# Performance work log

Measured on AMD Instinct MI355X. Metric: run time of the kernel, lower is better.

## Reference

```python
import jax, jax.numpy as jnp
import numpy as np

DIM = 1024
HEADS = 16
DH = DIM // HEADS          # 64
ROT_DIM = 2 * DH           # 128, rotary applied over concatenated x/a head dim
B, N = 2, 2048


def l2norm(t, eps=1e-12):
    # F.normalize(p=2, dim=-1)
    n = jnp.sqrt(jnp.sum(t * t, axis=-1, keepdims=True))
    return t / jnp.maximum(n, eps)


def rotate_half(t):
    t1, t2 = jnp.split(t, 2, axis=-1)
    return jnp.concatenate([-t2, t1], axis=-1)


def apply_rotary(q, k):
    # q: [b,h,n,ROT_DIM], k: [b,1,n,ROT_DIM]
    n = q.shape[-2]
    inv_freq = 1.0 / (10000.0 ** (jnp.arange(0, ROT_DIM, 2, dtype=jnp.float32) / ROT_DIM))
    freqs = jnp.outer(jnp.arange(n, dtype=jnp.float32), inv_freq)  # [n, ROT_DIM/2]
    emb = jnp.concatenate([freqs, freqs], axis=-1)                 # [n, ROT_DIM]
    cos, sin = jnp.cos(emb), jnp.sin(emb)
    q = q * cos + rotate_half(q) * sin
    k = k * cos + rotate_half(k) * sin
    return q, k


def setup_inputs() -> dict:
    key = jax.random.key(0)
    ks = jax.random.split(key, 6)
    s = 0.02
    return {
        "x": jax.random.normal(ks[0], (B, N, DIM), jnp.float32),
        "a": jax.random.normal(ks[1], (B, N, DIM), jnp.float32),
        "Wq_x": jax.random.normal(ks[2], (DIM, DIM), jnp.float32) * s,
        "Wkv_x": jax.random.normal(ks[3], (2 * DH, DIM), jnp.float32) * s,
        "Wq_a": jax.random.normal(ks[4], (DIM, DIM), jnp.float32) * s,
        "Wkv_a": jax.random.normal(ks[5], (2 * DH, DIM), jnp.float32) * s,
        "qx_scale": jnp.ones((HEADS, 1, DH), jnp.float32),
        "qa_scale": jnp.ones((HEADS, 1, DH), jnp.float32),
        "kx_scale": jnp.ones((1, 1, DH), jnp.float32),
        "ka_scale": jnp.ones((1, 1, DH), jnp.float32),
    }


def reference(x, a, Wq_x, Wkv_x, Wq_a, Wkv_a, qx_scale, qa_scale, kx_scale, ka_scale):
    b, n, _ = x.shape
    # q projections: [b,n,dim] -> [b,h,n,dh]
    q_x = (x @ Wq_x.T).reshape(b, n, HEADS, DH).transpose(0, 2, 1, 3)
    q_a = (a @ Wq_a.T).reshape(b, n, HEADS, DH).transpose(0, 2, 1, 3)
    # shared single KV head: [b,n,2*dh] -> two [b,1,n,dh]
    kv_x = x @ Wkv_x.T
    k_x, v_x = jnp.split(kv_x[:, None], 2, axis=-1)
    kv_a = a @ Wkv_a.T
    k_a, v_a = jnp.split(kv_a[:, None], 2, axis=-1)
    # qk-norm with learned per-head (q) / shared (k) scales
    q_x = l2norm(q_x) * qx_scale
    q_a = l2norm(q_a) * qa_scale
    k_x = l2norm(k_x) * kx_scale
    k_a = l2norm(k_a) * ka_scale
    # concat modalities along feature dim -> head dim 2*dh
    q = jnp.concatenate([q_x, q_a], axis=-1)   # [b,h,n,2dh]
    k = jnp.concatenate([k_x, k_a], axis=-1)   # [b,1,n,2dh]
    v = jnp.concatenate([v_x, v_a], axis=-1)   # [b,1,n,2dh]
    q, k = apply_rotary(q, k)
    # SDPA with broadcasted single KV head
    scale = 1.0 / jnp.sqrt(jnp.float32(ROT_DIM))
    k2, v2 = k[:, 0], v[:, 0]                  # [b,n,2dh]
    scores = jnp.einsum("bhqd,bkd->bhqk", q * scale, k2)
    attn = jax.nn.softmax(scores, axis=-1)
    out = jnp.einsum("bhqk,bkd->bhqd", attn, v2)  # [b,h,n,2dh]
    return out.transpose(0, 2, 1, 3).reshape(b, n, HEADS * ROT_DIM)
```

## Files before the change

kernel.cpp:

```cpp
#include <hip/hip_runtime.h>
#include <math.h>

#define DIM   1024
#define HEADS 16
#define DH    64
#define ROT   128
#define BATCH 2
#define SEQ   2048
#define ROWS  (BATCH*SEQ)
#define PCOLS (DIM + 2*DH)
#define ASCALE (0.08838834764831845f * 1.4426950408889634f)

typedef short bf16x8 __attribute__((ext_vector_type(8)));
typedef float f32x16 __attribute__((ext_vector_type(16)));
typedef unsigned u32x2 __attribute__((ext_vector_type(2)));

static __device__ __forceinline__ unsigned short f2bf(float f) {
    union { float f; unsigned u; } v; v.f = f;
    unsigned r = v.u + 0x7fffu + ((v.u >> 16) & 1u);
    return (unsigned short)(r >> 16);
}
static __device__ __forceinline__ float bf2f(unsigned short u) {
    union { unsigned u; float f; } v; v.u = (unsigned)u << 16;
    return v.f;
}

#define GL2LDS(gp, lp) __builtin_amdgcn_global_load_lds(                    \
    (const __attribute__((address_space(1))) void*)(gp),                    \
    (__attribute__((address_space(3))) void*)(lp), 16, 0, 0)
#define CFENCE() asm volatile("" ::: "memory")
#define WAIT_VM8()  __builtin_amdgcn_s_waitcnt(0xF78)
#define WAIT_VM0()  __builtin_amdgcn_s_waitcnt(0xF70)

__global__ __launch_bounds__(256) void convert_kernel(
    const float* __restrict__ x, const float* __restrict__ a,
    const float* __restrict__ Wq_x, const float* __restrict__ Wkv_x,
    const float* __restrict__ Wq_a, const float* __restrict__ Wkv_a,
    unsigned short* __restrict__ xbf, unsigned short* __restrict__ wbf,
    float2* __restrict__ tbl)
{
    const int blk = blockIdx.x;
    const float LN1E4_64 = 0.14391156831213f;
    if (blk >= 2624) {
        int local = blk - 2624;
        int pos = local * 16 + (threadIdx.x >> 4);
        int i   = threadIdx.x & 15;
        #pragma unroll
        for (int j = 0; j < 4; j++) {
            int jd = i * 4 + j;
            float th = (float)pos * expf(-LN1E4_64 * (float)jd);
            float sn, cs; sincosf(th, &sn, &cs);
            tbl[pos * 64 + jd] = make_float2(cs, sn);
        }
        return;
    }
    const float* s; unsigned short* d; int seg0;
    if      (blk < 1024) { s = x;     d = xbf;           seg0 = 0;    }
    else if (blk < 2048) { s = a;     d = xbf + 4194304; seg0 = 1024; }
    else if (blk < 2304) { s = Wq_x;  d = wbf;           seg0 = 2048; }
    else if (blk < 2336) { s = Wkv_x; d = wbf + 1048576; seg0 = 2304; }
    else if (blk < 2592) { s = Wq_a;  d = wbf + 1179648; seg0 = 2336; }
    else                 { s = Wkv_a; d = wbf + 2228224; seg0 = 2592; }
    long lb = ((long)blk - seg0) * 1024;
    #pragma unroll
    for (int j = 0; j < 4; j++) {
        long idx = lb + j * 256 + threadIdx.x;
        float4 v = ((const float4*)s)[idx];
        ((ushort4*)d)[idx] = make_ushort4(f2bf(v.x), f2bf(v.y), f2bf(v.z), f2bf(v.w));
    }
}

__global__ __launch_bounds__(256) void mfma_gemm_kernel(
    const unsigned short* __restrict__ xbf, const unsigned short* __restrict__ wbf,
    unsigned short* __restrict__ Pbf)
{
    const int mt = blockIdx.x, jt = blockIdx.y, side = blockIdx.z;
    const unsigned short* Ag = xbf + ((size_t)side * ROWS  + mt * 128) * DIM;
    const unsigned short* Bg = wbf + ((size_t)side * PCOLS + jt * 128) * DIM;
    unsigned short* Pp = Pbf + (size_t)side * ROWS * PCOLS;

    __shared__ __align__(16) unsigned short As[128 * 32];
    __shared__ __align__(16) unsigned short Bs[128 * 32];

    const int tid  = threadIdx.x;
    const int wave = tid >> 6, lane = tid & 63;
    const int m = lane & 31, hl = lane >> 5;
    const int wr = wave >> 1, wc = wave & 1;

    f32x16 acc[2][2];
    #pragma unroll
    for (int i2 = 0; i2 < 2; i2++)
        #pragma unroll
        for (int j2 = 0; j2 < 2; j2++) acc[i2][j2] = 0.0f;

    int sr[2], sg[2]; unsigned ldsb[2];
    #pragma unroll
    for (int it = 0; it < 2; it++) {
        int s = it * 256 + tid;
        sr[it] = s >> 2;
        sg[it] = (s & 3) ^ ((sr[it] >> 1) & 3);
        ldsb[it] = (unsigned)(it * 256 + wave * 64) * 16;
    }

    for (int k0 = 0; k0 < DIM; k0 += 32) {
        __syncthreads();
        #pragma unroll
        for (int it = 0; it < 2; it++) {
            GL2LDS(Ag + (size_t)sr[it] * DIM + k0 + sg[it] * 8, (char*)As + ldsb[it]);
            GL2LDS(Bg + (size_t)sr[it] * DIM + k0 + sg[it] * 8, (char*)Bs + ldsb[it]);
        }
        __syncthreads();
        #pragma unroll
        for (int kp = 0; kp < 2; kp++) {
            bf16x8 af[2], bff[2];
            #pragma unroll
            for (int t2 = 0; t2 < 2; t2++) {
                int ra = wr * 64 + t2 * 32 + m;
                int ga = (kp * 2 + hl) ^ ((ra >> 1) & 3);
                af[t2] = *(const bf16x8*)&As[ra * 32 + ga * 8];
                int rb = wc * 64 + t2 * 32 + m;
                int gb = (kp * 2 + hl) ^ ((rb >> 1) & 3);
                bff[t2] = *(const bf16x8*)&Bs[rb * 32 + gb * 8];
            }
            #pragma unroll
            for (int i2 = 0; i2 < 2; i2++)
                #pragma unroll
                for (int j2 = 0; j2 < 2; j2++)
                    acc[i2][j2] = __builtin_amdgcn_mfma_f32_32x32x16_bf16(
                        af[i2], bff[j2], acc[i2][j2], 0, 0, 0);
        }
    }

    const int m0 = mt * 128 + wr * 64;
    const int n0 = jt * 128 + wc * 64;
    #pragma unroll
    for (int i2 = 0; i2 < 2; i2++)
        #pragma unroll
        for (int j2 = 0; j2 < 2; j2++)
            #pragma unroll
            for (int r = 0; r < 16; r++) {
                int row = m0 + i2 * 32 + (r & 3) + 8 * (r >> 2) + 4 * hl;
                int col = n0 + j2 * 32 + m;
                Pp[(size_t)row * PCOLS + col] = f2bf(acc[i2][j2][r]);
            }
}

__global__ __launch_bounds__(256) void fuse_kernel(
    const unsigned short* __restrict__ Pbf,
    const float* __restrict__ qx_scale, const float* __restrict__ qa_scale,
    const float* __restrict__ kx_scale, const float* __restrict__ ka_scale,
    const float2* __restrict__ tbl,
    unsigned short* __restrict__ qbuf, unsigned short* __restrict__ kbuf,
    unsigned short* __restrict__ vbufT)
{
    const int row = blockIdx.x;
    const int b = row >> 11, pos = row & 2047;
    const unsigned short* Px = Pbf + (size_t)row * PCOLS;
    const unsigned short* Pa = Pbf + (size_t)ROWS * PCOLS + (size_t)row * PCOLS;
    const int tid = threadIdx.x;
    const int h = tid >> 4, i = tid & 15;
    const float2* tb = tbl + pos * 64;

    ushort4 xu = *(const ushort4*)(Px + h * DH + i * 4);
    ushort4 au = *(const ushort4*)(Pa + h * DH + i * 4);
    float xr[4] = {bf2f(xu.x), bf2f(xu.y), bf2f(xu.z), bf2f(xu.w)};
    float ar[4] = {bf2f(au.x), bf2f(au.y), bf2f(au.z), bf2f(au.w)};
    float ssx = xr[0]*xr[0] + xr[1]*xr[1] + xr[2]*xr[2] + xr[3]*xr[3];
    float ssa = ar[0]*ar[0] + ar[1]*ar[1] + ar[2]*ar[2] + ar[3]*ar[3];
    #pragma unroll
    for (int off = 1; off < 16; off <<= 1) {
        ssx += __shfl_xor(ssx, off, 16);
        ssa += __shfl_xor(ssa, off, 16);
    }
    float inx = 1.0f / fmaxf(sqrtf(ssx), 1e-12f);
    float ina = 1.0f / fmaxf(sqrtf(ssa), 1e-12f);
    unsigned short qlo[4], qhi[4];
    #pragma unroll
    for (int j = 0; j < 4; j++) {
        int jd = i * 4 + j;
        float qx = xr[j] * inx * qx_scale[h * DH + jd];
        float qa = ar[j] * ina * qa_scale[h * DH + jd];
        float2 cssn = tb[jd];
        qlo[j] = f2bf((qx * cssn.x - qa * cssn.y) * ASCALE);
        qhi[j] = f2bf((qa * cssn.x + qx * cssn.y) * ASCALE);
    }
    unsigned short* qp = qbuf + (((size_t)(b * HEADS + h)) * SEQ + pos) * ROT;
    *(ushort4*)(qp + i * 4)      = make_ushort4(qlo[0], qlo[1], qlo[2], qlo[3]);
    *(ushort4*)(qp + DH + i * 4) = make_ushort4(qhi[0], qhi[1], qhi[2], qhi[3]);

    if (tid < 16) {
        ushort4 kxu = *(const ushort4*)(Px + DIM + tid * 4);
        ushort4 kau = *(const ushort4*)(Pa + DIM + tid * 4);
        float kxr[4] = {bf2f(kxu.x), bf2f(kxu.y), bf2f(kxu.z), bf2f(kxu.w)};
        float kar[4] = {bf2f(kau.x), bf2f(kau.y), bf2f(kau.z), bf2f(kau.w)};
        float sx = kxr[0]*kxr[0] + kxr[1]*kxr[1] + kxr[2]*kxr[2] + kxr[3]*kxr[3];
        float sa = kar[0]*kar[0] + kar[1]*kar[1] + kar[2]*kar[2] + kar[3]*kar[3];
        #pragma unroll
        for (int off = 1; off < 16; off <<= 1) {
            sx += __shfl_xor(sx, off, 16);
            sa += __shfl_xor(sa, off, 16);
        }
        float ikx = 1.0f / fmaxf(sqrtf(sx), 1e-12f);
        float ika = 1.0f / fmaxf(sqrtf(sa), 1e-12f);
        unsigned short klo[4], khi[4];
        #pragma unroll
        for (int j = 0; j < 4; j++) {
            int jd = tid * 4 + j;
            float kx = kxr[j] * ikx * kx_scale[jd];
            float ka = kar[j] * ika * ka_scale[jd];
            float2 cssn = tb[jd];
            klo[j] = f2bf(kx * cssn.x - ka * cssn.y);
            khi[j] = f2bf(ka * cssn.x + kx * cssn.y);
        }
        unsigned short* kp = kbuf + ((size_t)b * SEQ + pos) * ROT;
        *(ushort4*)(kp + tid * 4)      = make_ushort4(klo[0], klo[1], klo[2], klo[3]);
        *(ushort4*)(kp + DH + tid * 4) = make_ushort4(khi[0], khi[1], khi[2], khi[3]);
    }
    if (tid >= 64 && tid < 96) {
        int iv = tid - 64;
        unsigned short* vT = vbufT + (size_t)b * ROT * SEQ + pos;
        const unsigned short* src; int d;
        if (iv < 16) { src = Px + DIM + DH + iv * 4;        d = iv * 4;              }
        else         { src = Pa + DIM + DH + (iv - 16) * 4; d = DH + (iv - 16) * 4;  }
        ushort4 v4 = *(const ushort4*)src;
        vT[(size_t)(d + 0) * SEQ] = v4.x;
        vT[(size_t)(d + 1) * SEQ] = v4.y;
        vT[(size_t)(d + 2) * SEQ] = v4.z;
        vT[(size_t)(d + 3) * SEQ] = v4.w;
    }
}

__global__ __launch_bounds__(256, 2) void attn_kernel(
    const unsigned short* __restrict__ qbuf,
    const unsigned short* __restrict__ kbuf,
    const unsigned short* __restrict__ vbufT,
    float* __restrict__ out)
{
    const int qb = blockIdx.x, h = blockIdx.y, b = blockIdx.z;
    __shared__ __align__(16) unsigned short smem[32768];
    const char* sc = (const char*)smem;
    const int tid  = threadIdx.x;
    const int wave = tid >> 6, lane = tid & 63;
    const int m = lane & 31, hl = lane >> 5;
    const int q0 = qb * 128 + wave * 32;

    bf16x8 qf[8];
    {
        const unsigned short* qp = qbuf + (((size_t)(b * HEADS + h)) * SEQ + q0 + m) * ROT + hl * 8;
        #pragma unroll
        for (int c = 0; c < 8; c++) qf[c] = *(const bf16x8*)(qp + c * 16);
    }

    f32x16 oacc[4];
    #pragma unroll
    for (int dt = 0; dt < 4; dt++) oacc[dt] = 0.0f;
    float lsum = 0.f;

    unsigned koff[8];
    #pragma unroll
    for (int c = 0; c < 8; c++)
        koff[c] = (unsigned)(m * 256 + (((2 * c + hl) ^ (m & 15)) << 4));
    unsigned voff[2][2];
    #pragma unroll
    for (int kg = 0; kg < 2; kg++)
        #pragma unroll
        for (int w = 0; w < 2; w++)
            voff[kg][w] = (unsigned)(32768 + m * 128 +
                                     (((kg * 4 + w * 2 + hl) ^ ((m >> 2) & 7)) << 4));

    const unsigned short* kb_ = kbuf  + (size_t)b * SEQ * ROT;
    const unsigned short* vb_ = vbufT + (size_t)b * ROT * SEQ;

    const unsigned short* ksrc[4];
    const unsigned short* vsrc[4];
    unsigned ldst[4];
    #pragma unroll
    for (int i = 0; i < 4; i++) {
        int fg = i * 256 + tid;
        int krow = fg >> 4, kgr = fg & 15;
        ksrc[i] = kb_ + (size_t)krow * ROT + ((kgr ^ (krow & 15)) << 3);
        int rv = fg >> 3, gv = fg & 7;
        vsrc[i] = vb_ + (size_t)rv * SEQ + ((gv ^ ((rv >> 2) & 7)) << 3);
        ldst[i] = (unsigned)(i * 256 + wave * 64) * 16;
    }

    #pragma unroll
    for (int i = 0; i < 4; i++) {
        GL2LDS(ksrc[i], sc + ldst[i]);
        GL2LDS(vsrc[i], sc + 32768 + ldst[i]);
    }

#define ATTN_TILE(BUF, T)                                                            \
  {                                                                                  \
    if ((T) < 31) {                          \
      _Pragma("unroll")                                                              \
      for (int i = 0; i < 4; i++) {                                                  \
        GL2LDS(ksrc[i] + (size_t)((T) + 1) * 64 * ROT,                               \
               sc + ((BUF) ^ 1) * 16384 + ldst[i]);                                  \
        GL2LDS(vsrc[i] + ((T) + 1) * 64,                                             \
               sc + 32768 + ((BUF) ^ 1) * 16384 + ldst[i]);                          \
      }                                                                              \
    }                                                                                \
    CFENCE();                                                                        \
    if ((T) < 31) WAIT_VM8(); else WAIT_VM0();      \
    __builtin_amdgcn_s_barrier();                                                    \
    CFENCE();                                                                        \
    f32x16 st0 = 0.0f, st1 = 0.0f;                                                   \
    __builtin_amdgcn_s_setprio(1);                                                   \
    _Pragma("unroll")                                                                \
    for (int c = 0; c < 8; c++) {                                                    \
      bf16x8 a0 = *(const bf16x8*)(sc + (BUF) * 16384 + koff[c]);                    \
      st0 = __builtin_amdgcn_mfma_f32_32x32x16_bf16(a0, qf[c], st0, 0, 0, 0);        \
    }                                                                                \
    _Pragma("unroll")                                                                \
    for (int c = 0; c < 8; c++) {                                                    \
      bf16x8 a1 = *(const bf16x8*)(sc + (BUF) * 16384 + 8192 + koff[c]);             \
      st1 = __builtin_amdgcn_mfma_f32_32x32x16_bf16(a1, qf[c], st1, 0, 0, 0);        \
    }                                                                                \
    __builtin_amdgcn_s_setprio(0);                                                   \
    _Pragma("unroll")                                                                \
    for (int kg = 0; kg < 2; kg++) {                                                 \
      float p[16];                                                                   \
      _Pragma("unroll")                                                              \
      for (int r = 0; r < 16; r++) {                                                 \
        float sv = kg ? st1[r] : st0[r];                                             \
        p[r] = __builtin_amdgcn_exp2f(sv); lsum += p[r];                             \
      }                                                                              \
      __builtin_amdgcn_s_setprio(1);                                                 \
      _Pragma("unroll")                                                              \
      for (int w = 0; w < 2; w++) {                                                  \
        unsigned pk0, pk1, pk2, pk3;                                                 \
        asm("v_cvt_pk_bf16_f32 %0, %1, %2" : "=v"(pk0) : "v"(p[8*w+0]), "v"(p[8*w+1])); \
        asm("v_cvt_pk_bf16_f32 %0, %1, %2" : "=v"(pk1) : "v"(p[8*w+2]), "v"(p[8*w+3])); \
        asm("v_cvt_pk_bf16_f32 %0, %1, %2" : "=v"(pk2) : "v"(p[8*w+4]), "v"(p[8*w+5])); \
        asm("v_cvt_pk_bf16_f32 %0, %1, %2" : "=v"(pk3) : "v"(p[8*w+6]), "v"(p[8*w+7])); \
        u32x2 s0 = __builtin_amdgcn_permlane32_swap(pk0, pk2, false, false);         \
        u32x2 s1 = __builtin_amdgcn_permlane32_swap(pk1, pk3, false, false);         \
        union { unsigned u[4]; bf16x8 v; } apu;                                      \
        apu.u[0] = s0[0]; apu.u[1] = s1[0]; apu.u[2] = s0[1]; apu.u[3] = s1[1];      \
        bf16x8 aP = apu.v;                                                           \
        _Pragma("unroll")                                                            \
        for (int dt = 0; dt < 4; dt++) {                                             \
          bf16x8 vf = *(const bf16x8*)(sc + (BUF) * 16384 + voff[kg][w] + dt * 4096);\
          oacc[dt] = __builtin_amdgcn_mfma_f32_32x32x16_bf16(aP, vf, oacc[dt], 0, 0, 0); \
        }                                                                            \
      }                                                                              \
      __builtin_amdgcn_s_setprio(0);                                                 \
    }                                                                                \
    CFENCE();                                                                        \
    __builtin_amdgcn_s_barrier();     \
    CFENCE();                                                                        \
  }

    for (int tt = 0; tt < 32; tt += 2) {
        ATTN_TILE(0, tt);
        ATTN_TILE(1, tt + 1);
    }
#undef ATTN_TILE

    lsum += __shfl_xor(lsum, 32);
    float* ob = out + ((size_t)(b * SEQ + q0)) * (HEADS * ROT) + h * ROT + m;
    #pragma unroll
    for (int r = 0; r < 16; r++) {
        int qrow = (r & 3) + 8 * (r >> 2) + 4 * hl;
        float linv = 1.0f / __shfl(lsum, qrow);
        float* orow = ob + (size_t)qrow * (HEADS * ROT);
        #pragma unroll
        for (int dt = 0; dt < 4; dt++) orow[dt * 32] = oacc[dt][r] * linv;
    }
}

extern "C" void kernel_launch(void* const* d_in, const int* in_sizes, int n_in,
                              void* d_out, int out_size, void* d_ws, size_t ws_size,
                              hipStream_t stream) {
    (void)in_sizes; (void)n_in; (void)out_size; (void)ws_size;
    const float* x        = (const float*)d_in[0];
    const float* a        = (const float*)d_in[1];
    const float* Wq_x     = (const float*)d_in[2];
    const float* Wkv_x    = (const float*)d_in[3];
    const float* Wq_a     = (const float*)d_in[4];
    const float* Wkv_a    = (const float*)d_in[5];
    const float* qx_scale = (const float*)d_in[6];
    const float* qa_scale = (const float*)d_in[7];
    const float* kx_scale = (const float*)d_in[8];
    const float* ka_scale = (const float*)d_in[9];
    float* out = (float*)d_out;

    unsigned short* Pbf   = (unsigned short*)d_ws;
    unsigned short* qbuf  = Pbf   + (size_t)2 * ROWS * PCOLS;
    unsigned short* kbuf  = qbuf  + (size_t)BATCH * HEADS * SEQ * ROT;
    unsigned short* vbufT = kbuf  + (size_t)BATCH * SEQ * ROT;
    unsigned short* xbf   = vbufT + (size_t)BATCH * SEQ * ROT;
    unsigned short* wbf   = xbf   + (size_t)2 * ROWS * DIM;
    float2*         tbl   = (float2*)(wbf + (size_t)2 * PCOLS * DIM);

    convert_kernel<<<dim3(2752), 256, 0, stream>>>(x, a, Wq_x, Wkv_x, Wq_a, Wkv_a,
                                                   xbf, wbf, tbl);
    mfma_gemm_kernel<<<dim3(32, 9, 2), 256, 0, stream>>>(xbf, wbf, Pbf);
    fuse_kernel<<<dim3(ROWS), 256, 0, stream>>>(Pbf, qx_scale, qa_scale, kx_scale, ka_scale,
                                                tbl, qbuf, kbuf, vbufT);
    attn_kernel<<<dim3(SEQ / 128, HEADS, BATCH), 256, 0, stream>>>(qbuf, kbuf, vbufT, out);
}
```

Baseline: 212.6 us.

## Double-buffer GEMM LDS loads and batch fuse kernel rows with coalesced V transpose

The projection GEMM now double-buffers its LDS tiles, issuing the global-to-LDS loads for the next K step before computing the current one. It waits on a partial vmcnt so memory latency overlaps with the MFMA work. Separately, the fuse kernel handles 8 rows per block and stages V in shared memory, so the transposed V writes become 16-byte vector stores instead of scattered 2-byte stores. This doubles the GEMM's LDS use and serializes 8 rows per block in the fuse kernel, which cuts its parallelism.

```diff
diff --git a/kernel.cpp b/kernel.cpp
--- a/kernel.cpp
+++ b/kernel.cpp
@@ -30,6 +30,7 @@
     (__attribute__((address_space(3))) void*)(lp), 16, 0, 0)
 #define CFENCE() asm volatile("" ::: "memory")
 #define WAIT_VM8()  __builtin_amdgcn_s_waitcnt(0xF78)
+#define WAIT_VM4()  __builtin_amdgcn_s_waitcnt(0xF74)
 #define WAIT_VM0()  __builtin_amdgcn_s_waitcnt(0xF70)
 
 __global__ __launch_bounds__(256) void convert_kernel(
@@ -79,8 +80,7 @@
     const unsigned short* Bg = wbf + ((size_t)side * PCOLS + jt * 128) * DIM;
     unsigned short* Pp = Pbf + (size_t)side * ROWS * PCOLS;
 
-    __shared__ __align__(16) unsigned short As[128 * 32];
-    __shared__ __align__(16) unsigned short Bs[128 * 32];
+    __shared__ __align__(16) char scg[32768];
 
     const int tid  = threadIdx.x;
     const int wave = tid >> 6, lane = tid & 63;
@@ -93,43 +93,77 @@
         #pragma unroll
         for (int j2 = 0; j2 < 2; j2++) acc[i2][j2] = 0.0f;
 
-    int sr[2], sg[2]; unsigned ldsb[2];
+    const unsigned short* Asrc[2];
+    const unsigned short* Bsrc[2];
+    unsigned ldsb[2];
     #pragma unroll
     for (int it = 0; it < 2; it++) {
         int s = it * 256 + tid;
-        sr[it] = s >> 2;
-        sg[it] = (s & 3) ^ ((sr[it] >> 1) & 3);
+        int sr = s >> 2;
+        int sg = (s & 3) ^ ((sr >> 1) & 3);
+        Asrc[it] = Ag + (size_t)sr * DIM + sg * 8;
+        Bsrc[it] = Bg + (size_t)sr * DIM + sg * 8;
         ldsb[it] = (unsigned)(it * 256 + wave * 64) * 16;
     }
 
-    for (int k0 = 0; k0 < DIM; k0 += 32) {
-        __syncthreads();
-        #pragma unroll
-        for (int it = 0; it < 2; it++) {
-            GL2LDS(Ag + (size_t)sr[it] * DIM + k0 + sg[it] * 8, (char*)As + ldsb[it]);
-            GL2LDS(Bg + (size_t)sr[it] * DIM + k0 + sg[it] * 8, (char*)Bs + ldsb[it]);
-        }
-        __syncthreads();
-        #pragma unroll
-        for (int kp = 0; kp < 2; kp++) {
-            bf16x8 af[2], bff[2];
-            #pragma unroll
-            for (int t2 = 0; t2 < 2; t2++) {
-                int ra = wr * 64 + t2 * 32 + m;
-                int ga = (kp * 2 + hl) ^ ((ra >> 1) & 3);
-                af[t2] = *(const bf16x8*)&As[ra * 32 + ga * 8];
-                int rb = wc * 64 + t2 * 32 + m;
-                int gb = (kp * 2 + hl) ^ ((rb >> 1) & 3);
-                bff[t2] = *(const bf16x8*)&Bs[rb * 32 + gb * 8];
-            }
-            #pragma unroll
-            for (int i2 = 0; i2 < 2; i2++)
-                #pragma unroll
-                for (int j2 = 0; j2 < 2; j2++)
-                    acc[i2][j2] = __builtin_amdgcn_mfma_f32_32x32x16_bf16(
-                        af[i2], bff[j2], acc[i2][j2], 0, 0, 0);
-        }
-    }
+    unsigned aoff[2][2], boff[2][2];
+    #pragma unroll
+    for (int kp = 0; kp < 2; kp++)
+        #pragma unroll
+        for (int t2 = 0; t2 < 2; t2++) {
+            int ra = wr * 64 + t2 * 32 + m;
+            int ga = (kp * 2 + hl) ^ ((ra >> 1) & 3);
+            aoff[kp][t2] = (unsigned)(ra * 64 + ga * 16);
+            int rb = wc * 64 + t2 * 32 + m;
+            int gb = (kp * 2 + hl) ^ ((rb >> 1) & 3);
+            boff[kp][t2] = (unsigned)(rb * 64 + gb * 16);
+        }
+
+    #pragma unroll
+    for (int it = 0; it < 2; it++) {
+        GL2LDS(Asrc[it], scg + ldsb[it]);
+        GL2LDS(Bsrc[it], scg + 16384 + ldsb[it]);
+    }
+
+#define GEMM_TILE(BUF, T)                                                          \
+  {                                                                                \
+    if ((T) < 31) {                        \
+      _Pragma("unroll")                                                            \
+      for (int it = 0; it < 2; it++) {                                             \
+        GL2LDS(Asrc[it] + ((T) + 1) * 32, scg + ((BUF) ^ 1) * 8192 + ldsb[it]);    \
+        GL2LDS(Bsrc[it] + ((T) + 1) * 32,                                          \
+               scg + 16384 + ((BUF) ^ 1) * 8192 + ldsb[it]);                       \
+      }                                                                            \
+    }                                                                              \
+    CFENCE();                                                                      \
+    if ((T) < 31) WAIT_VM4(); else WAIT_VM0();    \
+    __builtin_amdgcn_s_barrier();                                                  \
+    CFENCE();                                                                      \
+    _Pragma("unroll")                                                              \
+    for (int kp = 0; kp < 2; kp++) {                                               \
+      bf16x8 af[2], bff[2];                                                        \
+      _Pragma("unroll")                                                            \
+      for (int t2 = 0; t2 < 2; t2++) {                                             \
+        af[t2]  = *(const bf16x8*)(scg + (BUF) * 8192 + aoff[kp][t2]);             \
+        bff[t2] = *(const bf16x8*)(scg + 16384 + (BUF) * 8192 + boff[kp][t2]);     \
+      }                                                                            \
+      _Pragma("unroll")                                                            \
+      for (int i2 = 0; i2 < 2; i2++)                                               \
+        _Pragma("unroll")                                                          \
+        for (int j2 = 0; j2 < 2; j2++)                                             \
+          acc[i2][j2] = __builtin_amdgcn_mfma_f32_32x32x16_bf16(                   \
+              af[i2], bff[j2], acc[i2][j2], 0, 0, 0);                              \
+    }                                                                              \
+    CFENCE();                                                                      \
+    __builtin_amdgcn_s_barrier();             \
+    CFENCE();                                                                      \
+  }
+
+    for (int tt = 0; tt < 32; tt += 2) {
+        GEMM_TILE(0, tt);
+        GEMM_TILE(1, tt + 1);
+    }
+#undef GEMM_TILE
 
     const int m0 = mt * 128 + wr * 64;
     const int n0 = jt * 128 + wc * 64;
@@ -153,80 +187,91 @@
     unsigned short* __restrict__ qbuf, unsigned short* __restrict__ kbuf,
     unsigned short* __restrict__ vbufT)
 {
-    const int row = blockIdx.x;
-    const int b = row >> 11, pos = row & 2047;
-    const unsigned short* Px = Pbf + (size_t)row * PCOLS;
-    const unsigned short* Pa = Pbf + (size_t)ROWS * PCOLS + (size_t)row * PCOLS;
+    const int blk = blockIdx.x;
+    const int b = blk >> 8;
+    const int pos0 = (blk & 255) << 3;
+    __shared__ unsigned short Vs[8][128];
     const int tid = threadIdx.x;
     const int h = tid >> 4, i = tid & 15;
-    const float2* tb = tbl + pos * 64;
-
-    ushort4 xu = *(const ushort4*)(Px + h * DH + i * 4);
-    ushort4 au = *(const ushort4*)(Pa + h * DH + i * 4);
-    float xr[4] = {bf2f(xu.x), bf2f(xu.y), bf2f(xu.z), bf2f(xu.w)};
-    float ar[4] = {bf2f(au.x), bf2f(au.y), bf2f(au.z), bf2f(au.w)};
-    float ssx = xr[0]*xr[0] + xr[1]*xr[1] + xr[2]*xr[2] + xr[3]*xr[3];
-    float ssa = ar[0]*ar[0] + ar[1]*ar[1] + ar[2]*ar[2] + ar[3]*ar[3];
-    #pragma unroll
-    for (int off = 1; off < 16; off <<= 1) {
-        ssx += __shfl_xor(ssx, off, 16);
-        ssa += __shfl_xor(ssa, off, 16);
-    }
-    float inx = 1.0f / fmaxf(sqrtf(ssx), 1e-12f);
-    float ina = 1.0f / fmaxf(sqrtf(ssa), 1e-12f);
-    unsigned short qlo[4], qhi[4];
-    #pragma unroll
-    for (int j = 0; j < 4; j++) {
-        int jd = i * 4 + j;
-        float qx = xr[j] * inx * qx_scale[h * DH + jd];
-        float qa = ar[j] * ina * qa_scale[h * DH + jd];
-        float2 cssn = tb[jd];
-        qlo[j] = f2bf((qx * cssn.x - qa * cssn.y) * ASCALE);
-        qhi[j] = f2bf((qa * cssn.x + qx * cssn.y) * ASCALE);
-    }
-    unsigned short* qp = qbuf + (((size_t)(b * HEADS + h)) * SEQ + pos) * ROT;
-    *(ushort4*)(qp + i * 4)      = make_ushort4(qlo[0], qlo[1], qlo[2], qlo[3]);
-    *(ushort4*)(qp + DH + i * 4) = make_ushort4(qhi[0], qhi[1], qhi[2], qhi[3]);
-
-    if (tid < 16) {
-        ushort4 kxu = *(const ushort4*)(Px + DIM + tid * 4);
-        ushort4 kau = *(const ushort4*)(Pa + DIM + tid * 4);
-        float kxr[4] = {bf2f(kxu.x), bf2f(kxu.y), bf2f(kxu.z), bf2f(kxu.w)};
-        float kar[4] = {bf2f(kau.x), bf2f(kau.y), bf2f(kau.z), bf2f(kau.w)};
-        float sx = kxr[0]*kxr[0] + kxr[1]*kxr[1] + kxr[2]*kxr[2] + kxr[3]*kxr[3];
-        float sa = kar[0]*kar[0] + kar[1]*kar[1] + kar[2]*kar[2] + kar[3]*kar[3];
+
+    for (int rr = 0; rr < 8; rr++) {
+        const int pos = pos0 + rr;
+        const int row = b * SEQ + pos;
+        const unsigned short* Px = Pbf + (size_t)row * PCOLS;
+        const unsigned short* Pa = Pbf + (size_t)ROWS * PCOLS + (size_t)row * PCOLS;
+        const float2* tb = tbl + pos * 64;
+
+        ushort4 xu = *(const ushort4*)(Px + h * DH + i * 4);
+        ushort4 au = *(const ushort4*)(Pa + h * DH + i * 4);
+        float xr[4] = {bf2f(xu.x), bf2f(xu.y), bf2f(xu.z), bf2f(xu.w)};
+        float ar[4] = {bf2f(au.x), bf2f(au.y), bf2f(au.z), bf2f(au.w)};
+        float ssx = xr[0]*xr[0] + xr[1]*xr[1] + xr[2]*xr[2] + xr[3]*xr[3];
+        float ssa = ar[0]*ar[0] + ar[1]*ar[1] + ar[2]*ar[2] + ar[3]*ar[3];
         #pragma unroll
         for (int off = 1; off < 16; off <<= 1) {
-            sx += __shfl_xor(sx, off, 16);
-            sa += __shfl_xor(sa, off, 16);
-        }
-        float ikx = 1.0f / fmaxf(sqrtf(sx), 1e-12f);
-        float ika = 1.0f / fmaxf(sqrtf(sa), 1e-12f);
-        unsigned short klo[4], khi[4];
+            ssx += __shfl_xor(ssx, off, 16);
+            ssa += __shfl_xor(ssa, off, 16);
+        }
+        float inx = 1.0f / fmaxf(sqrtf(ssx), 1e-12f);
+        float ina = 1.0f / fmaxf(sqrtf(ssa), 1e-12f);
+        unsigned short qlo[4], qhi[4];
         #pragma unroll
         for (int j = 0; j < 4; j++) {
-            int jd = tid * 4 + j;
-            float kx = kxr[j] * ikx * kx_scale[jd];
-            float ka = kar[j] * ika * ka_scale[jd];
+            int jd = i * 4 + j;
+            float qx = xr[j] * inx * qx_scale[h * DH + jd];
+            float qa = ar[j] * ina * qa_scale[h * DH + jd];
             float2 cssn = tb[jd];
-            klo[j] = f2bf(kx * cssn.x - ka * cssn.y);
-            khi[j] = f2bf(ka * cssn.x + kx * cssn.y);
-        }
-        unsigned short* kp = kbuf + ((size_t)b * SEQ + pos) * ROT;
-        *(ushort4*)(kp + tid * 4)      = make_ushort4(klo[0], klo[1], klo[2], klo[3]);
-        *(ushort4*)(kp + DH + tid * 4) = make_ushort4(khi[0], khi[1], khi[2], khi[3]);
-    }
-    if (tid >= 64 && tid < 96) {
-        int iv = tid - 64;
-        unsigned short* vT = vbufT + (size_t)b * ROT * SEQ + pos;
-        const unsigned short* src; int d;
-        if (iv < 16) { src = Px + DIM + DH + iv * 4;        d = iv * 4;              }
-        else         { src = Pa + DIM + DH + (iv - 16) * 4; d = DH + (iv - 16) * 4;  }
-        ushort4 v4 = *(const ushort4*)src;
-        vT[(size_t)(d + 0) * SEQ] = v4.x;
-        vT[(size_t)(d + 1) * SEQ] = v4.y;
-        vT[(size_t)(d + 2) * SEQ] = v4.z;
-        vT[(size_t)(d + 3) * SEQ] = v4.w;
+            qlo[j] = f2bf((qx * cssn.x - qa * cssn.y) * ASCALE);
+            qhi[j] = f2bf((qa * cssn.x + qx * cssn.y) * ASCALE);
+        }
+        unsigned short* qp = qbuf + (((size_t)(b * HEADS + h)) * SEQ + pos) * ROT;
+        *(ushort4*)(qp + i * 4)      = make_ushort4(qlo[0], qlo[1], qlo[2], qlo[3]);
+        *(ushort4*)(qp + DH + i * 4) = make_ushort4(qhi[0], qhi[1], qhi[2], qhi[3]);
+
+        if (tid < 16) {
+            ushort4 kxu = *(const ushort4*)(Px + DIM + tid * 4);
+            ushort4 kau = *(const ushort4*)(Pa + DIM + tid * 4);
+            float kxr[4] = {bf2f(kxu.x), bf2f(kxu.y), bf2f(kxu.z), bf2f(kxu.w)};
+            float kar[4] = {bf2f(kau.x), bf2f(kau.y), bf2f(kau.z), bf2f(kau.w)};
+            float sx = kxr[0]*kxr[0] + kxr[1]*kxr[1] + kxr[2]*kxr[2] + kxr[3]*kxr[3];
+            float sa = kar[0]*kar[0] + kar[1]*kar[1] + kar[2]*kar[2] + kar[3]*kar[3];
+            #pragma unroll
+            for (int off = 1; off < 16; off <<= 1) {
+                sx += __shfl_xor(sx, off, 16);
+                sa += __shfl_xor(sa, off, 16);
+            }
+            float ikx = 1.0f / fmaxf(sqrtf(sx), 1e-12f);
+            float ika = 1.0f / fmaxf(sqrtf(sa), 1e-12f);
+            unsigned short klo[4], khi[4];
+            #pragma unroll
+            for (int j = 0; j < 4; j++) {
+                int jd = tid * 4 + j;
+                float kx = kxr[j] * ikx * kx_scale[jd];
+                float ka = kar[j] * ika * ka_scale[jd];
+                float2 cssn = tb[jd];
+                klo[j] = f2bf(kx * cssn.x - ka * cssn.y);
+                khi[j] = f2bf(ka * cssn.x + kx * cssn.y);
+            }
+            unsigned short* kp = kbuf + ((size_t)b * SEQ + pos) * ROT;
+            *(ushort4*)(kp + tid * 4)      = make_ushort4(klo[0], klo[1], klo[2], klo[3]);
+            *(ushort4*)(kp + DH + tid * 4) = make_ushort4(khi[0], khi[1], khi[2], khi[3]);
+        }
+        if (tid >= 64 && tid < 96) {
+            int iv = tid - 64;
+            const unsigned short* src; int d;
+            if (iv < 16) { src = Px + DIM + DH + iv * 4;        d = iv * 4;              }
+            else         { src = Pa + DIM + DH + (iv - 16) * 4; d = DH + (iv - 16) * 4;  }
+            ushort4 v4 = *(const ushort4*)src;
+            *(ushort4*)&Vs[rr][d] = v4;
+        }
+    }
+    __syncthreads();
+    if (tid < 128) {
+        const int d = tid;
+        union { unsigned short u[8]; bf16x8 v; } pk;
+        #pragma unroll
+        for (int rr = 0; rr < 8; rr++) pk.u[rr] = Vs[rr][d];
+        *(bf16x8*)(vbufT + (size_t)b * ROT * SEQ + (size_t)d * SEQ + pos0) = pk.v;
     }
 }
 
@@ -397,7 +442,7 @@
     convert_kernel<<<dim3(2752), 256, 0, stream>>>(x, a, Wq_x, Wkv_x, Wq_a, Wkv_a,
                                                    xbf, wbf, tbl);
     mfma_gemm_kernel<<<dim3(32, 9, 2), 256, 0, stream>>>(xbf, wbf, Pbf);
-    fuse_kernel<<<dim3(ROWS), 256, 0, stream>>>(Pbf, qx_scale, qa_scale, kx_scale, ka_scale,
-                                                tbl, qbuf, kbuf, vbufT);
+    fuse_kernel<<<dim3(ROWS / 8), 256, 0, stream>>>(Pbf, qx_scale, qa_scale, kx_scale, ka_scale,
+                                                    tbl, qbuf, kbuf, vbufT);
     attn_kernel<<<dim3(SEQ / 128, HEADS, BATCH), 256, 0, stream>>>(qbuf, kbuf, vbufT, out);
 }
```

Result: slower. 220.6 us (+3.8%).

## Fuse projection GEMM with qk-norm/rotary epilogue and restructure attention barriers

Applied to the files above, without the earlier changes.

Merges the bf16 projection GEMM and the separate normalize/rotary kernel into one kernel. Each block computes both the x and a sides sequentially over 64 K-steps, using double-buffered LDS and 8 waves. The l2norm, scale, rotary and V-transpose are applied directly from accumulators, so the intermediate Pbf round-trip and one launch go away. The attention tile loop also moves to a single wait-and-barrier at the start of each tile instead of a partial wait plus a trailing barrier. In exchange, the grid halves to 288 blocks, which may lower GPU occupancy, and the epilogue does strided scattered stores.

```diff
diff --git a/kernel.cpp b/kernel.cpp
--- a/kernel.cpp
+++ b/kernel.cpp
@@ -29,7 +29,6 @@
     (const __attribute__((address_space(1))) void*)(gp),                    \
     (__attribute__((address_space(3))) void*)(lp), 16, 0, 0)
 #define CFENCE() asm volatile("" ::: "memory")
-#define WAIT_VM8()  __builtin_amdgcn_s_waitcnt(0xF78)
 #define WAIT_VM0()  __builtin_amdgcn_s_waitcnt(0xF70)
 
 __global__ __launch_bounds__(256) void convert_kernel(
@@ -70,163 +69,150 @@
     }
 }
 
-__global__ __launch_bounds__(256) void mfma_gemm_kernel(
+__global__ __launch_bounds__(512) void gemm_fuse_kernel(
     const unsigned short* __restrict__ xbf, const unsigned short* __restrict__ wbf,
-    unsigned short* __restrict__ Pbf)
-{
-    const int mt = blockIdx.x, jt = blockIdx.y, side = blockIdx.z;
-    const unsigned short* Ag = xbf + ((size_t)side * ROWS  + mt * 128) * DIM;
-    const unsigned short* Bg = wbf + ((size_t)side * PCOLS + jt * 128) * DIM;
-    unsigned short* Pp = Pbf + (size_t)side * ROWS * PCOLS;
-
-    __shared__ __align__(16) unsigned short As[128 * 32];
-    __shared__ __align__(16) unsigned short Bs[128 * 32];
-
-    const int tid  = threadIdx.x;
-    const int wave = tid >> 6, lane = tid & 63;
-    const int m = lane & 31, hl = lane >> 5;
-    const int wr = wave >> 1, wc = wave & 1;
-
-    f32x16 acc[2][2];
-    #pragma unroll
-    for (int i2 = 0; i2 < 2; i2++)
-        #pragma unroll
-        for (int j2 = 0; j2 < 2; j2++) acc[i2][j2] = 0.0f;
-
-    int sr[2], sg[2]; unsigned ldsb[2];
-    #pragma unroll
-    for (int it = 0; it < 2; it++) {
-        int s = it * 256 + tid;
-        sr[it] = s >> 2;
-        sg[it] = (s & 3) ^ ((sr[it] >> 1) & 3);
-        ldsb[it] = (unsigned)(it * 256 + wave * 64) * 16;
-    }
-
-    for (int k0 = 0; k0 < DIM; k0 += 32) {
-        __syncthreads();
-        #pragma unroll
-        for (int it = 0; it < 2; it++) {
-            GL2LDS(Ag + (size_t)sr[it] * DIM + k0 + sg[it] * 8, (char*)As + ldsb[it]);
-            GL2LDS(Bg + (size_t)sr[it] * DIM + k0 + sg[it] * 8, (char*)Bs + ldsb[it]);
-        }
-        __syncthreads();
-        #pragma unroll
-        for (int kp = 0; kp < 2; kp++) {
-            bf16x8 af[2], bff[2];
-            #pragma unroll
-            for (int t2 = 0; t2 < 2; t2++) {
-                int ra = wr * 64 + t2 * 32 + m;
-                int ga = (kp * 2 + hl) ^ ((ra >> 1) & 3);
-                af[t2] = *(const bf16x8*)&As[ra * 32 + ga * 8];
-                int rb = wc * 64 + t2 * 32 + m;
-                int gb = (kp * 2 + hl) ^ ((rb >> 1) & 3);
-                bff[t2] = *(const bf16x8*)&Bs[rb * 32 + gb * 8];
-            }
-            #pragma unroll
-            for (int i2 = 0; i2 < 2; i2++)
-                #pragma unroll
-                for (int j2 = 0; j2 < 2; j2++)
-                    acc[i2][j2] = __builtin_amdgcn_mfma_f32_32x32x16_bf16(
-                        af[i2], bff[j2], acc[i2][j2], 0, 0, 0);
-        }
-    }
-
-    const int m0 = mt * 128 + wr * 64;
-    const int n0 = jt * 128 + wc * 64;
-    #pragma unroll
-    for (int i2 = 0; i2 < 2; i2++)
-        #pragma unroll
-        for (int j2 = 0; j2 < 2; j2++)
-            #pragma unroll
-            for (int r = 0; r < 16; r++) {
-                int row = m0 + i2 * 32 + (r & 3) + 8 * (r >> 2) + 4 * hl;
-                int col = n0 + j2 * 32 + m;
-                Pp[(size_t)row * PCOLS + col] = f2bf(acc[i2][j2][r]);
-            }
-}
-
-__global__ __launch_bounds__(256) void fuse_kernel(
-    const unsigned short* __restrict__ Pbf,
     const float* __restrict__ qx_scale, const float* __restrict__ qa_scale,
     const float* __restrict__ kx_scale, const float* __restrict__ ka_scale,
     const float2* __restrict__ tbl,
     unsigned short* __restrict__ qbuf, unsigned short* __restrict__ kbuf,
     unsigned short* __restrict__ vbufT)
 {
-    const int row = blockIdx.x;
-    const int b = row >> 11, pos = row & 2047;
-    const unsigned short* Px = Pbf + (size_t)row * PCOLS;
-    const unsigned short* Pa = Pbf + (size_t)ROWS * PCOLS + (size_t)row * PCOLS;
-    const int tid = threadIdx.x;
-    const int h = tid >> 4, i = tid & 15;
-    const float2* tb = tbl + pos * 64;
-
-    ushort4 xu = *(const ushort4*)(Px + h * DH + i * 4);
-    ushort4 au = *(const ushort4*)(Pa + h * DH + i * 4);
-    float xr[4] = {bf2f(xu.x), bf2f(xu.y), bf2f(xu.z), bf2f(xu.w)};
-    float ar[4] = {bf2f(au.x), bf2f(au.y), bf2f(au.z), bf2f(au.w)};
-    float ssx = xr[0]*xr[0] + xr[1]*xr[1] + xr[2]*xr[2] + xr[3]*xr[3];
-    float ssa = ar[0]*ar[0] + ar[1]*ar[1] + ar[2]*ar[2] + ar[3]*ar[3];
-    #pragma unroll
-    for (int off = 1; off < 16; off <<= 1) {
-        ssx += __shfl_xor(ssx, off, 16);
-        ssa += __shfl_xor(ssa, off, 16);
-    }
-    float inx = 1.0f / fmaxf(sqrtf(ssx), 1e-12f);
-    float ina = 1.0f / fmaxf(sqrtf(ssa), 1e-12f);
-    unsigned short qlo[4], qhi[4];
-    #pragma unroll
-    for (int j = 0; j < 4; j++) {
-        int jd = i * 4 + j;
-        float qx = xr[j] * inx * qx_scale[h * DH + jd];
-        float qa = ar[j] * ina * qa_scale[h * DH + jd];
-        float2 cssn = tb[jd];
-        qlo[j] = f2bf((qx * cssn.x - qa * cssn.y) * ASCALE);
-        qhi[j] = f2bf((qa * cssn.x + qx * cssn.y) * ASCALE);
-    }
-    unsigned short* qp = qbuf + (((size_t)(b * HEADS + h)) * SEQ + pos) * ROT;
-    *(ushort4*)(qp + i * 4)      = make_ushort4(qlo[0], qlo[1], qlo[2], qlo[3]);
-    *(ushort4*)(qp + DH + i * 4) = make_ushort4(qhi[0], qhi[1], qhi[2], qhi[3]);
-
-    if (tid < 16) {
-        ushort4 kxu = *(const ushort4*)(Px + DIM + tid * 4);
-        ushort4 kau = *(const ushort4*)(Pa + DIM + tid * 4);
-        float kxr[4] = {bf2f(kxu.x), bf2f(kxu.y), bf2f(kxu.z), bf2f(kxu.w)};
-        float kar[4] = {bf2f(kau.x), bf2f(kau.y), bf2f(kau.z), bf2f(kau.w)};
-        float sx = kxr[0]*kxr[0] + kxr[1]*kxr[1] + kxr[2]*kxr[2] + kxr[3]*kxr[3];
-        float sa = kar[0]*kar[0] + kar[1]*kar[1] + kar[2]*kar[2] + kar[3]*kar[3];
-        #pragma unroll
-        for (int off = 1; off < 16; off <<= 1) {
-            sx += __shfl_xor(sx, off, 16);
-            sa += __shfl_xor(sa, off, 16);
-        }
-        float ikx = 1.0f / fmaxf(sqrtf(sx), 1e-12f);
-        float ika = 1.0f / fmaxf(sqrtf(sa), 1e-12f);
-        unsigned short klo[4], khi[4];
-        #pragma unroll
-        for (int j = 0; j < 4; j++) {
-            int jd = tid * 4 + j;
-            float kx = kxr[j] * ikx * kx_scale[jd];
-            float ka = kar[j] * ika * ka_scale[jd];
-            float2 cssn = tb[jd];
-            klo[j] = f2bf(kx * cssn.x - ka * cssn.y);
-            khi[j] = f2bf(ka * cssn.x + kx * cssn.y);
-        }
-        unsigned short* kp = kbuf + ((size_t)b * SEQ + pos) * ROT;
-        *(ushort4*)(kp + tid * 4)      = make_ushort4(klo[0], klo[1], klo[2], klo[3]);
-        *(ushort4*)(kp + DH + tid * 4) = make_ushort4(khi[0], khi[1], khi[2], khi[3]);
-    }
-    if (tid >= 64 && tid < 96) {
-        int iv = tid - 64;
-        unsigned short* vT = vbufT + (size_t)b * ROT * SEQ + pos;
-        const unsigned short* src; int d;
-        if (iv < 16) { src = Px + DIM + DH + iv * 4;        d = iv * 4;              }
-        else         { src = Pa + DIM + DH + (iv - 16) * 4; d = DH + (iv - 16) * 4;  }
-        ushort4 v4 = *(const ushort4*)src;
-        vT[(size_t)(d + 0) * SEQ] = v4.x;
-        vT[(size_t)(d + 1) * SEQ] = v4.y;
-        vT[(size_t)(d + 2) * SEQ] = v4.z;
-        vT[(size_t)(d + 3) * SEQ] = v4.w;
+    const int mt = blockIdx.x, jt = blockIdx.y;
+    __shared__ __align__(16) char scg[32768];
+    const int tid  = threadIdx.x;
+    const int wave = tid >> 6, lane = tid & 63;
+    const int m = lane & 31, hl = lane >> 5;
+    const int wr = wave >> 1, wc = wave & 1;
+
+    f32x16 acc0[2], acc1[2];
+    acc0[0] = 0.0f; acc0[1] = 0.0f; acc1[0] = 0.0f; acc1[1] = 0.0f;
+
+    const int srow = tid >> 2;
+    const int sg   = (tid & 3) ^ ((srow >> 1) & 3);
+    const unsigned short* Asrc = xbf + (size_t)mt * 128 * DIM + (size_t)srow * DIM + sg * 8;
+    const unsigned short* Bsrc = wbf + (size_t)jt * 128 * DIM + (size_t)srow * DIM + sg * 8;
+    const unsigned ldsw = (unsigned)wave * 1024;
+
+    const int ra = wr * 32 + m;
+    unsigned aoff[2], boff[2][2];
+    #pragma unroll
+    for (int kp = 0; kp < 2; kp++) {
+        aoff[kp] = (unsigned)(ra * 64 + (((kp * 2 + hl) ^ ((ra >> 1) & 3)) << 4));
+        #pragma unroll
+        for (int j2 = 0; j2 < 2; j2++) {
+            int rb = wc * 64 + j2 * 32 + m;
+            boff[kp][j2] = (unsigned)(rb * 64 + (((kp * 2 + hl) ^ ((rb >> 1) & 3)) << 4));
+        }
+    }
+
+    GL2LDS(Asrc, scg + ldsw);
+    GL2LDS(Bsrc, scg + 16384 + ldsw);
+
+#define GEMM_STEP(ACC, BUF, T)                                                   \
+  {                                                                              \
+    CFENCE();                                                                    \
+    WAIT_VM0();                                                                  \
+    __builtin_amdgcn_s_barrier();                                                \
+    CFENCE();                                                                    \
+    if ((T) < 63) {                                                              \
+      const int nt = (T) + 1;                                                    \
+      const size_t so = (size_t)(nt >> 5);                                       \
+      const int kk = (nt & 31) * 32;                                             \
+      GL2LDS(Asrc + so * ((size_t)ROWS * DIM) + kk,                              \
+             scg + ((BUF) ^ 1) * 8192 + ldsw);                                   \
+      GL2LDS(Bsrc + so * ((size_t)PCOLS * DIM) + kk,                             \
+             scg + 16384 + ((BUF) ^ 1) * 8192 + ldsw);                           \
+    }                                                                            \
+    CFENCE();                                                                    \
+    _Pragma("unroll")                                                            \
+    for (int kp = 0; kp < 2; kp++) {                                             \
+      bf16x8 af = *(const bf16x8*)(scg + (BUF) * 8192 + aoff[kp]);               \
+      bf16x8 b0 = *(const bf16x8*)(scg + 16384 + (BUF) * 8192 + boff[kp][0]);    \
+      bf16x8 b1 = *(const bf16x8*)(scg + 16384 + (BUF) * 8192 + boff[kp][1]);    \
+      ACC[0] = __builtin_amdgcn_mfma_f32_32x32x16_bf16(af, b0, ACC[0], 0, 0, 0); \
+      ACC[1] = __builtin_amdgcn_mfma_f32_32x32x16_bf16(af, b1, ACC[1], 0, 0, 0); \
+    }                                                                            \
+  }
+
+    for (int tt = 0; tt < 32; tt += 2) { GEMM_STEP(acc0, 0, tt); GEMM_STEP(acc0, 1, tt + 1); }
+    for (int tt = 32; tt < 64; tt += 2) { GEMM_STEP(acc1, 0, tt); GEMM_STEP(acc1, 1, tt + 1); }
+#undef GEMM_STEP
+
+    const int rowbase = mt * 128 + wr * 32;
+    const int bb = rowbase >> 11;
+
+    if (jt < 8) {
+        const int h = jt * 2 + wc;
+        const float scx0 = qx_scale[h * DH + m], scx1 = qx_scale[h * DH + 32 + m];
+        const float sca0 = qa_scale[h * DH + m], sca1 = qa_scale[h * DH + 32 + m];
+        unsigned short* qbase = qbuf + ((size_t)(bb * HEADS + h)) * SEQ * ROT;
+        #pragma unroll
+        for (int r = 0; r < 16; r++) {
+            float px = acc0[0][r] * acc0[0][r] + acc0[1][r] * acc0[1][r];
+            float pa = acc1[0][r] * acc1[0][r] + acc1[1][r] * acc1[1][r];
+            #pragma unroll
+            for (int off = 1; off < 32; off <<= 1) {
+                px += __shfl_xor(px, off);
+                pa += __shfl_xor(pa, off);
+            }
+            float inx = 1.0f / fmaxf(sqrtf(px), 1e-12f);
+            float ina = 1.0f / fmaxf(sqrtf(pa), 1e-12f);
+            const int row = rowbase + (r & 3) + 8 * (r >> 2) + 4 * hl;
+            const int pos = row & 2047;
+            const float2* tp = tbl + pos * 64;
+            unsigned short* qrow = qbase + (size_t)pos * ROT;
+            #pragma unroll
+            for (int j2 = 0; j2 < 2; j2++) {
+                const int d = j2 * 32 + m;
+                float qx = acc0[j2][r] * inx * (j2 ? scx1 : scx0);
+                float qa = acc1[j2][r] * ina * (j2 ? sca1 : sca0);
+                float2 cs = tp[d];
+                qrow[d]      = f2bf((qx * cs.x - qa * cs.y) * ASCALE);
+                qrow[DH + d] = f2bf((qa * cs.x + qx * cs.y) * ASCALE);
+            }
+        }
+    } else if (wc == 0) {
+        const float scx0 = kx_scale[m], scx1 = kx_scale[32 + m];
+        const float sca0 = ka_scale[m], sca1 = ka_scale[32 + m];
+        unsigned short* kbase = kbuf + (size_t)bb * SEQ * ROT;
+        #pragma unroll
+        for (int r = 0; r < 16; r++) {
+            float px = acc0[0][r] * acc0[0][r] + acc0[1][r] * acc0[1][r];
+            float pa = acc1[0][r] * acc1[0][r] + acc1[1][r] * acc1[1][r];
+            #pragma unroll
+            for (int off = 1; off < 32; off <<= 1) {
+                px += __shfl_xor(px, off);
+                pa += __shfl_xor(pa, off);
+            }
+            float inx = 1.0f / fmaxf(sqrtf(px), 1e-12f);
+            float ina = 1.0f / fmaxf(sqrtf(pa), 1e-12f);
+            const int row = rowbase + (r & 3) + 8 * (r >> 2) + 4 * hl;
+            const int pos = row & 2047;
+            const float2* tp = tbl + pos * 64;
+            unsigned short* krow = kbase + (size_t)pos * ROT;
+            #pragma unroll
+            for (int j2 = 0; j2 < 2; j2++) {
+                const int d = j2 * 32 + m;
+                float kx = acc0[j2][r] * inx * (j2 ? scx1 : scx0);
+                float ka = acc1[j2][r] * ina * (j2 ? sca1 : sca0);
+                float2 cs = tp[d];
+                krow[d]      = f2bf(kx * cs.x - ka * cs.y);
+                krow[DH + d] = f2bf(ka * cs.x + kx * cs.y);
+            }
+        }
+    } else {
+        unsigned short* vb = vbufT + (size_t)bb * ROT * SEQ;
+        #pragma unroll
+        for (int r = 0; r < 16; r++) {
+            const int row = rowbase + (r & 3) + 8 * (r >> 2) + 4 * hl;
+            const int pos = row & 2047;
+            #pragma unroll
+            for (int j2 = 0; j2 < 2; j2++) {
+                const int d = j2 * 32 + m;
+                vb[(size_t)d * SEQ + pos]        = f2bf(acc0[j2][r]);
+                vb[(size_t)(DH + d) * SEQ + pos] = f2bf(acc1[j2][r]);
+            }
+        }
     }
 }
 
@@ -292,6 +278,10 @@
 
 #define ATTN_TILE(BUF, T)                                                            \
   {                                                                                  \
+    CFENCE();                                                                        \
+    WAIT_VM0();                                                                      \
+    __builtin_amdgcn_s_barrier();                                                    \
+    CFENCE();                                                                        \
     if ((T) < 31) {                          \
       _Pragma("unroll")                                                              \
       for (int i = 0; i < 4; i++) {                                                  \
@@ -301,9 +291,6 @@
                sc + 32768 + ((BUF) ^ 1) * 16384 + ldst[i]);                          \
       }                                                                              \
     }                                                                                \
-    CFENCE();                                                                        \
-    if ((T) < 31) WAIT_VM8(); else WAIT_VM0();      \
-    __builtin_amdgcn_s_barrier();                                                    \
     CFENCE();                                                                        \
     f32x16 st0 = 0.0f, st1 = 0.0f;                                                   \
     __builtin_amdgcn_s_setprio(1);                                                   \
@@ -347,9 +334,6 @@
       }                                                                              \
       __builtin_amdgcn_s_setprio(0);                                                 \
     }                                                                                \
-    CFENCE();                                                                        \
-    __builtin_amdgcn_s_barrier();     \
-    CFENCE();                                                                        \
   }
 
     for (int tt = 0; tt < 32; tt += 2) {
@@ -396,8 +380,8 @@
 
     convert_kernel<<<dim3(2752), 256, 0, stream>>>(x, a, Wq_x, Wkv_x, Wq_a, Wkv_a,
                                                    xbf, wbf, tbl);
-    mfma_gemm_kernel<<<dim3(32, 9, 2), 256, 0, stream>>>(xbf, wbf, Pbf);
-    fuse_kernel<<<dim3(ROWS), 256, 0, stream>>>(Pbf, qx_scale, qa_scale, kx_scale, ka_scale,
-                                                tbl, qbuf, kbuf, vbufT);
+    gemm_fuse_kernel<<<dim3(32, 9), 512, 0, stream>>>(xbf, wbf,
+                                                      qx_scale, qa_scale, kx_scale, ka_scale,
+                                                      tbl, qbuf, kbuf, vbufT);
     attn_kernel<<<dim3(SEQ / 128, HEADS, BATCH), 256, 0, stream>>>(qbuf, kbuf, vbufT, out);
 }
```

Result: slower. 217.0 us (+2.1%).
